# Kernel optimization log

Hardware: AMD Instinct MI355X
Metric: run time of the kernel (lower is better)

Reference implementation:

```python
import jax, jax.numpy as jnp
import numpy as np

N = 50000
E = 500000
IN_DIM = 128
HID = 128
EDGE_DIM = 1
MAX_DEPTH = 4  # depth values in [0, MAX_DEPTH]


def setup_inputs() -> dict:
    key = jax.random.key(0)
    ks = jax.random.split(key, 10)
    x = jax.random.normal(ks[0], (N, IN_DIM), jnp.float32)
    edge_index = jax.random.randint(ks[1], (2, E), 0, N)
    edge_attr = jax.random.normal(ks[2], (E, EDGE_DIM), jnp.float32)
    depth = jax.random.randint(ks[3], (N,), 0, MAX_DEPTH + 1)
    def w(k, sh):
        return (jax.random.normal(k, sh, jnp.float32) / np.float32(np.sqrt(sh[0])))
    return {
        "x": x, "edge_index": edge_index, "edge_attr": edge_attr, "depth": depth,
        "pw": w(ks[4], (IN_DIM, HID)), "pb": jnp.zeros((HID,), jnp.float32),
        "mw1": w(ks[5], (HID + EDGE_DIM, HID)), "mb1": jnp.zeros((HID,), jnp.float32),
        "mw2": w(ks[6], (HID, HID)), "mb2": jnp.zeros((HID,), jnp.float32),
        "uw1": w(ks[7], (2 * HID, HID)), "ub1": jnp.zeros((HID,), jnp.float32),
        "uw2": w(ks[8], (HID, HID)), "ub2": jnp.zeros((HID,), jnp.float32),
    }


def reference(x, edge_index, edge_attr, depth, pw, pb, mw1, mb1, mw2, mb2, uw1, ub1, uw2, ub2):
    src, dst = edge_index[0], edge_index[1]
    dst_depth = depth[dst]  # [E]
    h = x @ pw + pb  # node_proj -> [N, HID]
    # Sequential topological DP over depth levels (static unroll, small count).
    for d in range(1, MAX_DEPTH + 1):
        emask = dst_depth == d  # [E]
        # msg_mlp over all edges using current h (lower-depth nodes already updated)
        msg_in = jnp.concatenate([h[src], edge_attr], axis=-1)  # [E, HID+EDGE_DIM]
        msgs = jax.nn.relu(jax.nn.relu(msg_in @ mw1 + mb1) @ mw2 + mb2)
        msgs = jnp.where(emask[:, None], msgs, jnp.zeros((), h.dtype))
        agg = jax.ops.segment_sum(msgs, dst, num_segments=N)  # [N, HID]
        counts = jax.ops.segment_sum(emask.astype(h.dtype), dst, num_segments=N)
        agg = agg / jnp.clip(counts, 1.0)[:, None]  # mean aggregation, clamp(min=1)
        upd_in = jnp.concatenate([h, agg], axis=-1)  # [N, 2*HID]
        h_new = jax.nn.relu(jax.nn.relu(upd_in @ uw1 + ub1) @ uw2 + ub2)
        h = jnp.where((depth == d)[:, None], h_new, h)
    return h
```

## Files before the change

### kernel.cpp

```cpp
#include <hip/hip_runtime.h>

typedef _Float16 f16;
typedef f16 f16x2 __attribute__((ext_vector_type(2)));
typedef f16 f16x8 __attribute__((ext_vector_type(8)));
typedef float f32x4 __attribute__((ext_vector_type(4)));
typedef float f32x2 __attribute__((ext_vector_type(2)));

#define MFMA16(a, b, c) __builtin_amdgcn_mfma_f32_16x16x32_f16((a), (b), (c), 0, 0, 0)

static __device__ __forceinline__ f16x8 cvt8(const float* __restrict__ p) {
    f32x4 p0 = *(const f32x4*)p;
    f32x4 p1 = *(const f32x4*)(p + 4);
    f16x8 a;
    a[0] = (f16)p0[0]; a[1] = (f16)p0[1]; a[2] = (f16)p0[2]; a[3] = (f16)p0[3];
    a[4] = (f16)p1[0]; a[5] = (f16)p1[1]; a[6] = (f16)p1[2]; a[7] = (f16)p1[3];
    return a;
}

__global__ __launch_bounds__(256) void k_prep(
        const float* __restrict__ pw, const float* __restrict__ mw1,
        const float* __restrict__ mw2, const float* __restrict__ uw1,
        const float* __restrict__ uw2,
        f16* __restrict__ pwp, f16* __restrict__ mw1p, f16* __restrict__ mw2p,
        f16* __restrict__ uw1p, f16* __restrict__ uw2p,
        const int* __restrict__ ei, int* __restrict__ degv,
        const int* __restrict__ dep, int* __restrict__ dcnt,
        int4* __restrict__ recs, int CB, int E, int N) {
    __shared__ int lcnt[4];
    __shared__ int lbase[4];
    int b = blockIdx.x;
    int t = threadIdx.x;
    if (b < 48) {
        const float* W; f16* out; int fb;
        if (b < 8)       { W = pw;  out = pwp;  fb = b; }
        else if (b < 16) { W = mw1; out = mw1p; fb = b - 8; }
        else if (b < 24) { W = mw2; out = mw2p; fb = b - 16; }
        else if (b < 40) { W = uw1; out = uw1p; fb = b - 24; }
        else             { W = uw2; out = uw2p; fb = b - 40; }
        int idx = fb * 256 + t;
        int lane = idx & 63;
        int nt = (idx >> 6) & 7;
        int kt = idx >> 9;
        int colx = lane & 15, quad = lane >> 4;
        f16* o = out + (size_t)idx * 8;
        const float* wb = W + (size_t)(kt * 32 + quad * 8) * 128 + nt * 16 + colx;
#pragma unroll
        for (int j = 0; j < 8; j++) o[j] = (f16)wb[(size_t)j * 128];
    } else if (b < 48 + CB) {
        int e = (b - 48) * 256 + t;
        if (e < E) atomicAdd(&degv[ei[E + e]], 1);
    } else {
        if (t < 4) lcnt[t] = 0;
        __syncthreads();
        int v = (b - 48 - CB) * 256 + t;
        int d = (v < N) ? dep[v] : 0;
        int p = -1;
        if (d >= 1 && d <= 4) p = atomicAdd(&lcnt[d - 1], 1);
        __syncthreads();
        if (t < 4) lbase[t] = (lcnt[t] > 0) ? atomicAdd(&dcnt[t], lcnt[t]) : 0;
        __syncthreads();
        if (d >= 1 && d <= 4) recs[(size_t)(d - 1) * N + lbase[d - 1] + p].x = v;
    }
}

__global__ __launch_bounds__(256) void k_mid(
        const int* __restrict__ degv, int* __restrict__ bsum, int SB,
        const float* __restrict__ x, const f16* __restrict__ pwp,
        const f16* __restrict__ mw1p, const float* __restrict__ pb,
        const float* __restrict__ mb1, float* __restrict__ h,
        f16* __restrict__ hh, f16* __restrict__ t, int N) {
    __shared__ __align__(16) f16 lds[4][16 * 136];
    __shared__ int wsum[4];
    int tid = threadIdx.x;
    if ((int)blockIdx.x < SB) {
        int idx = blockIdx.x * 256 + tid;
        int v = (idx < N) ? degv[idx] : 0;
#pragma unroll
        for (int off = 32; off; off >>= 1) v += __shfl_down(v, off, 64);
        if ((tid & 63) == 0) wsum[tid >> 6] = v;
        __syncthreads();
        if (tid == 0) bsum[blockIdx.x] = wsum[0] + wsum[1] + wsum[2] + wsum[3];
        return;
    }
    int lane = tid & 63, w = tid >> 6;
    int colx = lane & 15, quad = lane >> 4;
    int base = ((blockIdx.x - SB) * 4 + w) * 16;
    int arow = base + colx;
    int u = arow < N ? arow : N - 1;

    f32x4 c1[8];
#pragma unroll
    for (int nt = 0; nt < 8; nt++) c1[nt] = (f32x4){0.f, 0.f, 0.f, 0.f};
#pragma unroll
    for (int kt = 0; kt < 4; kt++) {
        f16x8 a = cvt8(x + (size_t)u * 128 + kt * 32 + quad * 8);
#pragma unroll
        for (int nt = 0; nt < 8; nt++) {
            f16x8 b = *(const f16x8*)(pwp + ((size_t)(kt * 8 + nt) * 64 + lane) * 8);
            c1[nt] = MFMA16(a, b, c1[nt]);
        }
    }
#pragma unroll
    for (int nt = 0; nt < 8; nt++) {
        float bias = pb[nt * 16 + colx];
#pragma unroll
        for (int reg = 0; reg < 4; reg++) {
            int row = quad * 4 + reg;
            int node = base + row;
            float v = c1[nt][reg] + bias;
            lds[w][row * 136 + nt * 16 + colx] = (f16)v;
            if (node < N) {
                h[(size_t)node * 128 + nt * 16 + colx] = v;
                hh[(size_t)node * 128 + nt * 16 + colx] = (f16)v;
            }
        }
    }
    f32x4 c2[8];
#pragma unroll
    for (int nt = 0; nt < 8; nt++) c2[nt] = (f32x4){0.f, 0.f, 0.f, 0.f};
#pragma unroll
    for (int kt = 0; kt < 4; kt++) {
        f16x8 a = *(const f16x8*)&lds[w][colx * 136 + kt * 32 + quad * 8];
#pragma unroll
        for (int nt = 0; nt < 8; nt++) {
            f16x8 b = *(const f16x8*)(mw1p + ((size_t)(kt * 8 + nt) * 64 + lane) * 8);
            c2[nt] = MFMA16(a, b, c2[nt]);
        }
    }
#pragma unroll
    for (int nt = 0; nt < 8; nt++) {
        float bias = mb1[nt * 16 + colx];
#pragma unroll
        for (int reg = 0; reg < 4; reg++) {
            int node = base + quad * 4 + reg;
            if (node < N) t[(size_t)node * 128 + nt * 16 + colx] = (f16)(c2[nt][reg] + bias);
        }
    }
}

__global__ __launch_bounds__(256) void k_scanC(const int* __restrict__ degv,
                                               const int* __restrict__ bsum,
                                               int* __restrict__ rowp, int N, int E) {
    __shared__ int lds[256];
    __shared__ int wo[4];
    int b = blockIdx.x, t = threadIdx.x;
    int idx = b * 256 + t;
    int v = (idx < N) ? degv[idx] : 0;
    lds[t] = v;
    __syncthreads();
#pragma unroll
    for (int d = 1; d < 256; d <<= 1) {
        int u = (t >= d) ? lds[t - d] : 0;
        __syncthreads();
        lds[t] += u;
        __syncthreads();
    }
    int off = 0;
    for (int j = t; j < b; j += 256) off += bsum[j];
#pragma unroll
    for (int o = 32; o; o >>= 1) off += __shfl_down(off, o, 64);
    if ((t & 63) == 0) wo[t >> 6] = off;
    __syncthreads();
    int boff = wo[0] + wo[1] + wo[2] + wo[3];
    if (idx < N) rowp[idx] = boff + lds[t] - v;
    if (b == 0 && t == 0) rowp[N] = E;
}

__global__ __launch_bounds__(256) void k_scat(const int* __restrict__ ei,
                                              const float* __restrict__ eattr,
                                              const int* __restrict__ dep,
                                              const int* __restrict__ rowp,
                                              int* __restrict__ cur,
                                              int2* __restrict__ esea,
                                              int4* __restrict__ recs,
                                              const int* __restrict__ dcnt,
                                              int E, int N) {
    int gtid = blockIdx.x * 256 + threadIdx.x;
    int gsz = gridDim.x * 256;
    for (int e = gtid; e < E; e += gsz) {
        int s = ei[e], d = ei[E + e];
        int p = rowp[d] + atomicAdd(&cur[d], 1);
        esea[p] = (int2){s | (dep[s] << 20), __float_as_int(eattr[e])};
    }
    for (int d4 = 0; d4 < 4; d4++) {
        int cnt = dcnt[d4];
        for (int i = gtid; i < cnt; i += gsz) {
            int4* r = &recs[(size_t)d4 * N + i];
            int u = r->x;
            r->y = rowp[u];
            r->z = rowp[u + 1];
        }
    }
}

__global__ __launch_bounds__(256) void k_md(
        const f16* __restrict__ tOrg, f16* __restrict__ tUpd,
        const float* __restrict__ mw1, const float* __restrict__ mb2,
        const f16* __restrict__ mw2p, const int2* __restrict__ esea,
        const int4* __restrict__ recs, const int* __restrict__ dcnt,
        const f16* __restrict__ hh, const f16* __restrict__ uw1p,
        const f16* __restrict__ uw2p, const f16* __restrict__ mw1p,
        const float* __restrict__ ub1, const float* __restrict__ ub2,
        const float* __restrict__ mb1, float* __restrict__ h,
        int dIdx, int N) {
    __shared__ __align__(16) f16 bsm[128 * 128];
    __shared__ __align__(16) f16 pool[16][136];
    __shared__ __align__(16) f16 sout[16][136];
    __shared__ int ids[16];
    {
        const f16x8* s8 = (const f16x8*)mw2p;
        f16x8* d8 = (f16x8*)bsm;
        for (int i = threadIdx.x; i < 2048; i += 256) d8[i] = s8[i];
    }
    if (threadIdx.x < 16) ids[threadIdx.x] = 0;
    __syncthreads();

    const int tid = threadIdx.x;
    const int lane = tid & 63;
    const int w = tid >> 6;
    const int colx = lane & 15, quad = lane >> 4;
    const int cnt = dcnt[dIdx];

    const float* w1r = mw1 + 128 * 128;
    f16x8 w1h[4];
#pragma unroll
    for (int kt = 0; kt < 4; kt++) {
        f32x4 q0 = *(const f32x4*)(w1r + kt * 32 + quad * 8);
        f32x4 q1 = *(const f32x4*)(w1r + kt * 32 + quad * 8 + 4);
        w1h[kt][0] = (f16)q0[0]; w1h[kt][1] = (f16)q0[1];
        w1h[kt][2] = (f16)q0[2]; w1h[kt][3] = (f16)q0[3];
        w1h[kt][4] = (f16)q1[0]; w1h[kt][5] = (f16)q1[1];
        w1h[kt][6] = (f16)q1[2]; w1h[kt][7] = (f16)q1[3];
    }
    float mb2v[8];
#pragma unroll
    for (int nt = 0; nt < 8; nt++) mb2v[nt] = mb2[nt * 16 + colx];

    struct Pre { int u, e0, e1; f16 eah; f16x8 tv[4]; };
    auto srow = [&](int sv) -> const f16* {
        const f16* tb = ((unsigned)((sv >> 20) - 1) < (unsigned)dIdx) ? tUpd : tOrg;
        return tb + (size_t)(sv & 0xFFFFF) * 128;
    };
    auto load_pre = [&](int n) {
        Pre p;
        int4 r = recs[(size_t)dIdx * N + n];
        p.u = r.x; p.e0 = r.y; p.e1 = r.z;
        int lim = p.e1 - 1; if (lim < 0) lim = 0;
        int es = p.e0 + colx; if (es > lim) es = lim;
        int2 er = esea[es];
        p.eah = (f16)__int_as_float(er.y);
        const f16* trow = srow(er.x);
#pragma unroll
        for (int kt = 0; kt < 4; kt++)
            p.tv[kt] = *(const f16x8*)(trow + kt * 32 + quad * 8);
        return p;
    };
    auto build_afr = [&](const f16x8* tv, f16 eah, f16x8* afr) {
#pragma unroll
        for (int kt = 0; kt < 4; kt++) {
            f16x8 v = tv[kt];
            f16x8 o;
#pragma unroll
            for (int j = 0; j < 8; j++) {
                f16 q = v[j] + eah * w1h[kt][j];
                o[j] = q > (f16)0 ? q : (f16)0;
            }
            afr[kt] = o;
        }
    };
    auto tile_acc = [&](f16x8* afr, int bs, int e1, float* aggv) {
#pragma unroll
        for (int nt = 0; nt < 8; nt++) {
            f32x4 c = (f32x4){0.f, 0.f, 0.f, 0.f};
#pragma unroll
            for (int kt = 0; kt < 4; kt++) {
                f16x8 b = *(const f16x8*)&bsm[((kt * 8 + nt) * 64 + lane) * 8];
                c = MFMA16(afr[kt], b, c);
            }
#pragma unroll
            for (int reg = 0; reg < 4; reg++)
                if (bs + quad * 4 + reg < e1) aggv[nt] += fmaxf(c[reg] + mb2v[nt], 0.f);
        }
    };
    auto process = [&](const Pre& p, int r) {
        float aggv[8] = {0.f, 0.f, 0.f, 0.f, 0.f, 0.f, 0.f, 0.f};
        f16x8 afr[4];
        build_afr(p.tv, p.eah, afr);
        tile_acc(afr, p.e0, p.e1, aggv);
        for (int bs = p.e0 + 16; bs < p.e1; bs += 16) {
            int lim = p.e1 - 1;
            int es = bs + colx; if (es > lim) es = lim;
            int2 er = esea[es];
            f16 eah = (f16)__int_as_float(er.y);
            const f16* trow = srow(er.x);
            f16x8 tv[4];
#pragma unroll
            for (int kt = 0; kt < 4; kt++)
                tv[kt] = *(const f16x8*)(trow + kt * 32 + quad * 8);
            build_afr(tv, eah, afr);
            tile_acc(afr, bs, p.e1, aggv);
        }
        int deg = p.e1 - p.e0;
        float inv = 1.f / (float)(deg > 1 ? deg : 1);
#pragma unroll
        for (int nt = 0; nt < 8; nt++) {
            float s = aggv[nt];
            s += __shfl_xor(s, 16, 64);
            s += __shfl_xor(s, 32, 64);
            if (quad == 0) pool[r][nt * 16 + colx] = (f16)(s * inv);
        }
        if (lane == 0) ids[r] = p.u;
    };

    const int b = blockIdx.x, nb = gridDim.x;
    const int s0 = (int)((long long)cnt * b / nb);
    const int s1 = (int)((long long)cnt * (b + 1) / nb);

    for (int cs = s0; cs < s1; cs += 16) {
        int cc = s1 - cs; if (cc > 16) cc = 16;
        for (int rr = w; rr < cc; rr += 8) {
            Pre p0 = load_pre(cs + rr);
            if (rr + 4 < cc) {
                Pre p1 = load_pre(cs + rr + 4);
                process(p0, rr);
                process(p1, rr + 4);
            } else {
                process(p0, rr);
            }
        }
        __syncthreads();
        int arid = ids[colx];
        f32x4 c1[2];
        c1[0] = (f32x4){0.f, 0.f, 0.f, 0.f};
        c1[1] = (f32x4){0.f, 0.f, 0.f, 0.f};
#pragma unroll
        for (int kt = 0; kt < 8; kt++) {
            f16x8 a;
            if (kt < 4)
                a = *(const f16x8*)(hh + (size_t)arid * 128 + kt * 32 + quad * 8);
            else
                a = *(const f16x8*)&pool[colx][(kt - 4) * 32 + quad * 8];
#pragma unroll
            for (int j = 0; j < 2; j++) {
                int nt = 2 * w + j;
                f16x8 bb = *(const f16x8*)(uw1p + ((size_t)(kt * 8 + nt) * 64 + lane) * 8);
                c1[j] = MFMA16(a, bb, c1[j]);
            }
        }
#pragma unroll
        for (int j = 0; j < 2; j++) {
            int nt = 2 * w + j;
            float bias = ub1[nt * 16 + colx];
#pragma unroll
            for (int reg = 0; reg < 4; reg++) {
                int row = quad * 4 + reg;
                sout[row][nt * 16 + colx] = (f16)fmaxf(c1[j][reg] + bias, 0.f);
            }
        }
        __syncthreads();
        f32x4 c2[2];
        c2[0] = (f32x4){0.f, 0.f, 0.f, 0.f};
        c2[1] = (f32x4){0.f, 0.f, 0.f, 0.f};
#pragma unroll
        for (int kt = 0; kt < 4; kt++) {
            f16x8 a = *(const f16x8*)&sout[colx][kt * 32 + quad * 8];
#pragma unroll
            for (int j = 0; j < 2; j++) {
                int nt = 2 * w + j;
                f16x8 bb = *(const f16x8*)(uw2p + ((size_t)(kt * 8 + nt) * 64 + lane) * 8);
                c2[j] = MFMA16(a, bb, c2[j]);
            }
        }
#pragma unroll
        for (int j = 0; j < 2; j++) {
            int nt = 2 * w + j;
            float bias = ub2[nt * 16 + colx];
#pragma unroll
            for (int reg = 0; reg < 4; reg++) {
                int row = quad * 4 + reg;
                float v = fmaxf(c2[j][reg] + bias, 0.f);
                pool[row][nt * 16 + colx] = (f16)v;
                if (row < cc)
                    h[(size_t)ids[row] * 128 + nt * 16 + colx] = v;
            }
        }
        __syncthreads();
        if (dIdx < 3) {
            f32x4 c3[2];
            c3[0] = (f32x4){0.f, 0.f, 0.f, 0.f};
            c3[1] = (f32x4){0.f, 0.f, 0.f, 0.f};
#pragma unroll
            for (int kt = 0; kt < 4; kt++) {
                f16x8 a = *(const f16x8*)&pool[colx][kt * 32 + quad * 8];
#pragma unroll
                for (int j = 0; j < 2; j++) {
                    int nt = 2 * w + j;
                    f16x8 bb = *(const f16x8*)(mw1p + ((size_t)(kt * 8 + nt) * 64 + lane) * 8);
                    c3[j] = MFMA16(a, bb, c3[j]);
                }
            }
#pragma unroll
            for (int j = 0; j < 2; j++) {
                int nt = 2 * w + j;
                float bias = mb1[nt * 16 + colx];
#pragma unroll
                for (int reg = 0; reg < 4; reg++) {
                    int row = quad * 4 + reg;
                    if (row < cc)
                        tUpd[(size_t)ids[row] * 128 + nt * 16 + colx] = (f16)(c3[j][reg] + bias);
                }
            }
        }
        __syncthreads();
    }
}

extern "C" void kernel_launch(void* const* d_in, const int* in_sizes, int n_in,
                              void* d_out, int out_size, void* d_ws, size_t ws_size,
                              hipStream_t stream) {
    const float* x    = (const float*)d_in[0];
    const int*   ei   = (const int*)d_in[1];
    const float* eatt = (const float*)d_in[2];
    const int*   dep  = (const int*)d_in[3];
    const float* pw   = (const float*)d_in[4];
    const float* pb   = (const float*)d_in[5];
    const float* mw1  = (const float*)d_in[6];
    const float* mb1  = (const float*)d_in[7];
    const float* mw2  = (const float*)d_in[8];
    const float* mb2  = (const float*)d_in[9];
    const float* uw1  = (const float*)d_in[10];
    const float* ub1  = (const float*)d_in[11];
    const float* uw2  = (const float*)d_in[12];
    const float* ub2  = (const float*)d_in[13];
    float* h = (float*)d_out;

    int N = in_sizes[3];
    int E = in_sizes[1] / 2;
    int NB = (N + 255) / 256;
    int CB = (E + 255) / 256;

    char* ws = (char*)d_ws;
    size_t o = 0;
    auto alloc = [&](size_t bytes) -> char* {
        char* p = ws + o;
        o += (bytes + 255) & ~(size_t)255;
        return p;
    };
    f16*   t    = (f16*)alloc((size_t)N * 128 * 2);
    f16*   hh   = (f16*)alloc((size_t)N * 128 * 2);
    f16*   tUpd = (f16*)alloc((size_t)N * 128 * 2);
    char*  z0   = (char*)alloc(0);
    int*   degv = (int*)alloc((size_t)N * 4);
    int*   cur  = (int*)alloc((size_t)N * 4);
    int*   dcnt = (int*)alloc(64);
    size_t zbytes = (size_t)((char*)alloc(0) - z0);
    int*   rowp = (int*)alloc((size_t)(N + 1) * 4);
    int*   bsum = (int*)alloc((size_t)NB * 4);
    int2*  esea = (int2*)alloc((size_t)E * 8);
    int4*  recs = (int4*)alloc((size_t)4 * N * 16);
    f16*   pwp  = (f16*)alloc(128 * 128 * 2);
    f16*   mw1p = (f16*)alloc(128 * 128 * 2);
    f16*   mw2p = (f16*)alloc(128 * 128 * 2);
    f16*   uw1p = (f16*)alloc(256 * 128 * 2);
    f16*   uw2p = (f16*)alloc(128 * 128 * 2);

    hipMemsetAsync(z0, 0, zbytes, stream);

    k_prep<<<48 + CB + NB, 256, 0, stream>>>(pw, mw1, mw2, uw1, uw2,
                                             pwp, mw1p, mw2p, uw1p, uw2p,
                                             ei, degv, dep, dcnt, recs, CB, E, N);
    int PB = (N + 63) / 64;
    k_mid<<<NB + PB, 256, 0, stream>>>(degv, bsum, NB, x, pwp, mw1p, pb, mb1,
                                       h, hh, t, N);
    k_scanC<<<NB, 256, 0, stream>>>(degv, bsum, rowp, N, E);
    k_scat<<<CB, 256, 0, stream>>>(ei, eatt, dep, rowp, cur, esea, recs, dcnt, E, N);

    for (int d = 0; d < 4; d++) {
        k_md<<<768, 256, 0, stream>>>(t, tUpd, mw1, mb2, mw2p, esea, recs, dcnt,
                                      hh, uw1p, uw2p, mw1p, ub1, ub2, mb1, h,
                                      d, N);
    }
}
```

Baseline: 348.3 us.

## Stage gathered source rows in LDS cooperatively before MFMA edge processing

Replaces the per-wave register prefetch of source rows with a block-cooperative gather: edge records are staged into shared memory, then all 256 threads load 16-byte segments of source rows into an LDS tile buffer before each wave runs its MFMA message tile. Hidden rows for the update MLP are also staged through LDS, and the grid shrinks from 768 to 512 blocks. The aim is more coalesced, better-parallelised gathers, at the cost of extra block-wide barriers per 16-edge round, lockstep processing of four nodes bounded by the largest degree, and more LDS per block, which lowers occupancy.

Result: no change. 341.9 us (-1.8%).

```diff
diff --git a/kernel.cpp b/kernel.cpp
--- a/kernel.cpp
+++ b/kernel.cpp
@@ -204,16 +204,16 @@
         const float* __restrict__ mb1, float* __restrict__ h,
         int dIdx, int N) {
     __shared__ __align__(16) f16 bsm[128 * 128];
+    __shared__ __align__(16) f16 tbuf[4][16][136];
+    __shared__ int2 ebuf[4][16];
     __shared__ __align__(16) f16 pool[16][136];
     __shared__ __align__(16) f16 sout[16][136];
-    __shared__ int ids[16];
+    __shared__ int ids[16], se0[16], se1[16];
     {
         const f16x8* s8 = (const f16x8*)mw2p;
         f16x8* d8 = (f16x8*)bsm;
         for (int i = threadIdx.x; i < 2048; i += 256) d8[i] = s8[i];
     }
-    if (threadIdx.x < 16) ids[threadIdx.x] = 0;
-    __syncthreads();
 
     const int tid = threadIdx.x;
     const int lane = tid & 63;
@@ -236,100 +236,116 @@
 #pragma unroll
     for (int nt = 0; nt < 8; nt++) mb2v[nt] = mb2[nt * 16 + colx];
 
-    struct Pre { int u, e0, e1; f16 eah; f16x8 tv[4]; };
-    auto srow = [&](int sv) -> const f16* {
-        const f16* tb = ((unsigned)((sv >> 20) - 1) < (unsigned)dIdx) ? tUpd : tOrg;
-        return tb + (size_t)(sv & 0xFFFFF) * 128;
-    };
-    auto load_pre = [&](int n) {
-        Pre p;
-        int4 r = recs[(size_t)dIdx * N + n];
-        p.u = r.x; p.e0 = r.y; p.e1 = r.z;
-        int lim = p.e1 - 1; if (lim < 0) lim = 0;
-        int es = p.e0 + colx; if (es > lim) es = lim;
-        int2 er = esea[es];
-        p.eah = (f16)__int_as_float(er.y);
-        const f16* trow = srow(er.x);
-#pragma unroll
-        for (int kt = 0; kt < 4; kt++)
-            p.tv[kt] = *(const f16x8*)(trow + kt * 32 + quad * 8);
-        return p;
-    };
-    auto build_afr = [&](const f16x8* tv, f16 eah, f16x8* afr) {
-#pragma unroll
-        for (int kt = 0; kt < 4; kt++) {
-            f16x8 v = tv[kt];
-            f16x8 o;
-#pragma unroll
-            for (int j = 0; j < 8; j++) {
-                f16 q = v[j] + eah * w1h[kt][j];
-                o[j] = q > (f16)0 ? q : (f16)0;
-            }
-            afr[kt] = o;
-        }
-    };
-    auto tile_acc = [&](f16x8* afr, int bs, int e1, float* aggv) {
-#pragma unroll
-        for (int nt = 0; nt < 8; nt++) {
-            f32x4 c = (f32x4){0.f, 0.f, 0.f, 0.f};
-#pragma unroll
-            for (int kt = 0; kt < 4; kt++) {
-                f16x8 b = *(const f16x8*)&bsm[((kt * 8 + nt) * 64 + lane) * 8];
-                c = MFMA16(afr[kt], b, c);
-            }
-#pragma unroll
-            for (int reg = 0; reg < 4; reg++)
-                if (bs + quad * 4 + reg < e1) aggv[nt] += fmaxf(c[reg] + mb2v[nt], 0.f);
-        }
-    };
-    auto process = [&](const Pre& p, int r) {
-        float aggv[8] = {0.f, 0.f, 0.f, 0.f, 0.f, 0.f, 0.f, 0.f};
-        f16x8 afr[4];
-        build_afr(p.tv, p.eah, afr);
-        tile_acc(afr, p.e0, p.e1, aggv);
-        for (int bs = p.e0 + 16; bs < p.e1; bs += 16) {
-            int lim = p.e1 - 1;
-            int es = bs + colx; if (es > lim) es = lim;
-            int2 er = esea[es];
-            f16 eah = (f16)__int_as_float(er.y);
-            const f16* trow = srow(er.x);
-            f16x8 tv[4];
-#pragma unroll
-            for (int kt = 0; kt < 4; kt++)
-                tv[kt] = *(const f16x8*)(trow + kt * 32 + quad * 8);
-            build_afr(tv, eah, afr);
-            tile_acc(afr, bs, p.e1, aggv);
-        }
-        int deg = p.e1 - p.e0;
-        float inv = 1.f / (float)(deg > 1 ? deg : 1);
-#pragma unroll
-        for (int nt = 0; nt < 8; nt++) {
-            float s = aggv[nt];
-            s += __shfl_xor(s, 16, 64);
-            s += __shfl_xor(s, 32, 64);
-            if (quad == 0) pool[r][nt * 16 + colx] = (f16)(s * inv);
-        }
-        if (lane == 0) ids[r] = p.u;
-    };
-
     const int b = blockIdx.x, nb = gridDim.x;
     const int s0 = (int)((long long)cnt * b / nb);
     const int s1 = (int)((long long)cnt * (b + 1) / nb);
+    f16* hb = &tbuf[0][0][0];
+
+    __syncthreads();
 
     for (int cs = s0; cs < s1; cs += 16) {
         int cc = s1 - cs; if (cc > 16) cc = 16;
-        for (int rr = w; rr < cc; rr += 8) {
-            Pre p0 = load_pre(cs + rr);
-            if (rr + 4 < cc) {
-                Pre p1 = load_pre(cs + rr + 4);
-                process(p0, rr);
-                process(p1, rr + 4);
+        if (tid < 16) {
+            if (tid < cc) {
+                int4 r = recs[(size_t)dIdx * N + cs + tid];
+                ids[tid] = r.x; se0[tid] = r.y; se1[tid] = r.z;
             } else {
-                process(p0, rr);
-            }
-        }
-        __syncthreads();
-        int arid = ids[colx];
+                ids[tid] = 0; se0[tid] = 0; se1[tid] = 0;
+            }
+        }
+        __syncthreads();
+
+        for (int q = 0; q < 4; q++) {
+            int maxT = 0;
+#pragma unroll
+            for (int s = 0; s < 4; s++) {
+                int r = q * 4 + s;
+                int tc = (se1[r] - se0[r] + 15) >> 4;
+                if (tc > maxT) maxT = tc;
+            }
+            float aggv[8] = {0.f, 0.f, 0.f, 0.f, 0.f, 0.f, 0.f, 0.f};
+            for (int rd = 0; rd < maxT; rd++) {
+                if (tid < 64) {
+                    int s = tid >> 4, j = tid & 15;
+                    int r = q * 4 + s;
+                    int es = se0[r] + rd * 16 + j;
+                    if (es < se1[r]) ebuf[s][j] = esea[es];
+                }
+                __syncthreads();
+#pragma unroll
+                for (int it = 0; it < 4; it++) {
+                    int task = it * 256 + tid;
+                    int row = task >> 4, seg = task & 15;
+                    int s = row >> 4, j = row & 15;
+                    int r = q * 4 + s;
+                    int es = se0[r] + rd * 16 + j;
+                    if (es < se1[r]) {
+                        int sv = ebuf[s][j].x;
+                        const f16* tb =
+                            ((unsigned)((sv >> 20) - 1) < (unsigned)dIdx) ? tUpd : tOrg;
+                        *(f16x8*)&tbuf[s][j][seg * 8] =
+                            *(const f16x8*)(tb + (size_t)(sv & 0xFFFFF) * 128 + seg * 8);
+                    }
+                }
+                __syncthreads();
+                {
+                    int r = q * 4 + w;
+                    int bs = se0[r] + rd * 16;
+                    int rem = se1[r] - bs;
+                    if (rem > 0) {
+                        f16 eah = (f16)__int_as_float(ebuf[w][colx].y);
+                        f16x8 afr[4];
+#pragma unroll
+                        for (int kt = 0; kt < 4; kt++) {
+                            f16x8 v = *(const f16x8*)&tbuf[w][colx][kt * 32 + quad * 8];
+                            f16x8 o;
+#pragma unroll
+                            for (int j2 = 0; j2 < 8; j2++) {
+                                f16 qv = v[j2] + eah * w1h[kt][j2];
+                                o[j2] = qv > (f16)0 ? qv : (f16)0;
+                            }
+                            afr[kt] = o;
+                        }
+#pragma unroll
+                        for (int nt = 0; nt < 8; nt++) {
+                            f32x4 c = (f32x4){0.f, 0.f, 0.f, 0.f};
+#pragma unroll
+                            for (int kt = 0; kt < 4; kt++) {
+                                f16x8 bb = *(const f16x8*)&bsm[((kt * 8 + nt) * 64 + lane) * 8];
+                                c = MFMA16(afr[kt], bb, c);
+                            }
+#pragma unroll
+                            for (int reg = 0; reg < 4; reg++)
+                                if (quad * 4 + reg < rem)
+                                    aggv[nt] += fmaxf(c[reg] + mb2v[nt], 0.f);
+                        }
+                    }
+                }
+                __syncthreads();
+            }
+            {
+                int r = q * 4 + w;
+                int deg = se1[r] - se0[r];
+                float inv = 1.f / (float)(deg > 1 ? deg : 1);
+#pragma unroll
+                for (int nt = 0; nt < 8; nt++) {
+                    float s = aggv[nt];
+                    s += __shfl_xor(s, 16, 64);
+                    s += __shfl_xor(s, 32, 64);
+                    if (quad == 0) pool[r][nt * 16 + colx] = (f16)(s * inv);
+                }
+            }
+        }
+        __syncthreads();
+
+        {
+            int row = tid >> 4, seg = tid & 15;
+            if (row < cc)
+                *(f16x8*)&hb[row * 136 + seg * 8] =
+                    *(const f16x8*)(hh + (size_t)ids[row] * 128 + seg * 8);
+        }
+        __syncthreads();
+
         f32x4 c1[2];
         c1[0] = (f32x4){0.f, 0.f, 0.f, 0.f};
         c1[1] = (f32x4){0.f, 0.f, 0.f, 0.f};
@@ -337,7 +353,7 @@
         for (int kt = 0; kt < 8; kt++) {
             f16x8 a;
             if (kt < 4)
-                a = *(const f16x8*)(hh + (size_t)arid * 128 + kt * 32 + quad * 8);
+                a = *(const f16x8*)&hb[colx * 136 + kt * 32 + quad * 8];
             else
                 a = *(const f16x8*)&pool[colx][(kt - 4) * 32 + quad * 8];
 #pragma unroll
@@ -407,7 +423,8 @@
                 for (int reg = 0; reg < 4; reg++) {
                     int row = quad * 4 + reg;
                     if (row < cc)
-                        tUpd[(size_t)ids[row] * 128 + nt * 16 + colx] = (f16)(c3[j][reg] + bias);
+                        tUpd[(size_t)ids[row] * 128 + nt * 16 + colx] =
+                            (f16)(c3[j][reg] + bias);
                 }
             }
         }
@@ -476,7 +493,7 @@
     k_scat<<<CB, 256, 0, stream>>>(ei, eatt, dep, rowp, cur, esea, recs, dcnt, E, N);
 
     for (int d = 0; d < 4; d++) {
-        k_md<<<768, 256, 0, stream>>>(t, tUpd, mw1, mb2, mw2p, esea, recs, dcnt,
+        k_md<<<512, 256, 0, stream>>>(t, tUpd, mw1, mb2, mw2p, esea, recs, dcnt,
                                       hh, uw1p, uw2p, mw1p, ub1, ub2, mb1, h,
                                       d, N);
     }
```
